# Performance work log

Hardware: AMD Instinct MI355X
Metric: run time of the kernel (lower is better)

## Reference

```python
import jax, jax.numpy as jnp
import numpy as np

NUM_HEADS = 4


def setup_inputs() -> dict:
    key = jax.random.key(0)
    ks = jax.random.split(key, 12)
    N, E_edges, ND, ED, D, G = 50000, 800000, 128, 64, 256, 128
    h = jax.random.normal(ks[0], (N, ND), dtype=jnp.float32)
    edge_index = jax.random.randint(ks[1], (2, E_edges), 0, N)
    edge_attr = jax.random.normal(ks[2], (E_edges, ED), dtype=jnp.float32)
    batch = jnp.sort(jax.random.randint(ks[3], (N,), 0, G))
    node_w = jax.random.normal(ks[4], (D, ND), dtype=jnp.float32) / np.sqrt(ND)
    node_b = jnp.zeros((D,), dtype=jnp.float32)
    edge_w = jax.random.normal(ks[5], (D, ED), dtype=jnp.float32) / np.sqrt(ED)
    edge_b = jnp.zeros((D,), dtype=jnp.float32)
    query = jax.random.normal(ks[6], (1, D), dtype=jnp.float32)
    in_w = jax.random.normal(ks[7], (3 * D, D), dtype=jnp.float32) / np.sqrt(D)
    in_b = jnp.zeros((3 * D,), dtype=jnp.float32)
    out_w = jax.random.normal(ks[8], (D, D), dtype=jnp.float32) / np.sqrt(D)
    out_b = jnp.zeros((D,), dtype=jnp.float32)
    return {"h": h, "edge_index": edge_index, "edge_attr": edge_attr, "batch": batch,
            "num_graphs": G, "node_w": node_w, "node_b": node_b,
            "edge_w": edge_w, "edge_b": edge_b, "query": query,
            "in_w": in_w, "in_b": in_b, "out_w": out_w, "out_b": out_b}


def reference(h, edge_index, edge_attr, batch, num_graphs,
              node_w, node_b, edge_w, edge_b, query, in_w, in_b, out_w, out_b):
    N = h.shape[0]
    D = query.shape[-1]
    dh = D // NUM_HEADS
    G = num_graphs
    # node projection
    h_proj = h @ node_w.T + node_b  # [N, D]
    # scatter-mean edge features to source nodes
    row = edge_index[0]
    e_proj = edge_attr @ edge_w.T + edge_b  # [E, D]
    e_sum = jax.ops.segment_sum(e_proj, row, num_segments=N)
    cnt = jax.ops.segment_sum(jnp.ones((row.shape[0],), jnp.float32), row, num_segments=N)
    h_proj = h_proj + e_sum / jnp.maximum(cnt, 1.0)[:, None]
    # per-graph single-query multi-head attention (torch MultiheadAttention math)
    wq, wk, wv = in_w[:D], in_w[D:2 * D], in_w[2 * D:]
    bq, bk, bv = in_b[:D], in_b[D:2 * D], in_b[2 * D:]
    q = (query @ wq.T + bq).reshape(NUM_HEADS, dh)            # [H, dh]
    k = (h_proj @ wk.T + bk).reshape(N, NUM_HEADS, dh)        # [N, H, dh]
    v = (h_proj @ wv.T + bv).reshape(N, NUM_HEADS, dh)        # [N, H, dh]
    scores = jnp.einsum('hd,nhd->nh', q, k) / jnp.sqrt(jnp.float32(dh))  # [N, H]
    smax = jax.ops.segment_max(scores, batch, num_segments=G)  # [G, H]
    w = jnp.exp(scores - smax[batch])                          # [N, H]
    denom = jax.ops.segment_sum(w, batch, num_segments=G)      # [G, H]
    p = w / jnp.maximum(denom[batch], 1e-30)                   # [N, H]
    pooled = jax.ops.segment_sum(p[:, :, None] * v, batch, num_segments=G)  # [G, H, dh]
    out = pooled.reshape(G, 1, D) @ out_w.T + out_b            # [G, 1, D]
    return out
```

## Files before the change

kernel.cpp:

```cpp
#include <hip/hip_runtime.h>
#include <hip/hip_bf16.h>
#include <math.h>

#define NDIM 128
#define EDIM 64
#define DDIM 256
#define BM 32
#define APK_STRIDE 204
#define HPB_STRIDE 264
#define NSPLIT 4
#define CAP 96
#define NSWZ (8 * 12 * 64 * 8)

typedef __attribute__((ext_vector_type(8))) short short8;
typedef __attribute__((ext_vector_type(16))) float floatx16;

__device__ inline ushort f2bf(float x) {
    uint32_t u = __float_as_uint(x);
    uint32_t r = (u + 0x7fff + ((u >> 16) & 1)) >> 16;
    return (ushort)r;
}
__device__ inline float bf2f(ushort h) { return __uint_as_float(((uint32_t)h) << 16); }
__device__ inline uint32_t pack_hilo(float x) {
    ushort hi = f2bf(x);
    ushort lo = f2bf(x - bf2f(hi));
    return (uint32_t)hi | ((uint32_t)lo << 16);
}

__global__ __launch_bounds__(256) void k_setup(
    int* __restrict__ zero_p, int n_zero, int ZBLK,
    const float* __restrict__ node_w, const float* __restrict__ edge_w,
    ushort* __restrict__ whi, ushort* __restrict__ wlo,
    const float* __restrict__ query, const float* __restrict__ in_w,
    const float* __restrict__ in_b, float* __restrict__ qk, float* __restrict__ sb)
{
    const int tid = threadIdx.x;
    int b = blockIdx.x;
    if (b < ZBLK) {
        int i = b * 256 + tid;
        if (i < n_zero) zero_p[i] = 0;
        return;
    }
    b -= ZBLK;
    if (b < 192) {
        int idx = b * 256 + tid;
        int i = idx & 7;
        int l = (idx >> 3) & 63;
        int rest = idx >> 9;
        int s = rest % 12;
        int t2 = rest / 12;
        int k = s * 16 + (l >> 5) * 8 + i;
        int col = t2 * 32 + (l & 31);
        float val = (k < NDIM) ? node_w[(size_t)col * NDIM + k]
                               : edge_w[(size_t)col * EDIM + (k - NDIM)];
        ushort hi = f2bf(val);
        ushort lo = f2bf(val - bf2f(hi));
        whi[idx] = hi;
        wlo[idx] = lo;
        return;
    }
    __shared__ float q_s[DDIM];
    __shared__ float qv[DDIM];
    q_s[tid] = query[tid];
    __syncthreads();
    float acc = in_b[tid];
    const float* wq = in_w + (size_t)tid * DDIM;
    for (int i = 0; i < DDIM; ++i) acc += q_s[i] * wq[i];
    qv[tid] = acc;
    __syncthreads();
    for (int h = 0; h < 4; ++h) {
        float a = 0.f;
        for (int d = 0; d < 64; ++d)
            a += qv[h * 64 + d] * in_w[(size_t)(DDIM + h * 64 + d) * DDIM + tid];
        qk[h * DDIM + tid] = a;
    }
    if (tid < 4) {
        float a = 0.f;
        for (int d = 0; d < 64; ++d) a += qv[tid * 64 + d] * in_b[DDIM + tid * 64 + d];
        sb[tid] = a;
    }
}

__global__ __launch_bounds__(256) void k_scatter(
    const int* __restrict__ erow, int* __restrict__ fill,
    int* __restrict__ perm, int E)
{
    int e = blockIdx.x * 256 + threadIdx.x;
    if (e < E) {
        int r = erow[e];
        int pos = atomicAdd(&fill[r], 1);
        if (pos < CAP) perm[(size_t)r * CAP + pos] = e;
    }
}

__global__ __launch_bounds__(256) void k_projagg(
    const float* __restrict__ h, const float* __restrict__ edge_attr,
    const int* __restrict__ perm, const int* __restrict__ fill,
    const ushort* __restrict__ whi, const ushort* __restrict__ wlo,
    const float* __restrict__ node_b, const float* __restrict__ edge_b,
    const float* __restrict__ qk, const float* __restrict__ sb,
    ushort* __restrict__ h_proj_bf, float* __restrict__ scores, int N)
{
    extern __shared__ char smem[];
    uint32_t* A_pk = (uint32_t*)smem;
    ushort*   hpbuf = (ushort*)smem;
    __shared__ float qk_s[4 * DDIM];
    __shared__ float cnt_s[BM];
    __shared__ float sb_s[4];

    const int tid = threadIdx.x;
    const int n0 = blockIdx.x * BM;

    if (tid < BM) {
        int n = n0 + tid;
        cnt_s[tid] = (n < N) ? (float)fill[n] : 0.f;
    }
    if (tid < 4) sb_s[tid] = sb[tid];
    for (int i = tid; i < 4 * DDIM; i += 256) qk_s[i] = qk[i];

    const float4* h4 = reinterpret_cast<const float4*>(h);
#pragma unroll
    for (int it = 0; it < 4; ++it) {
        int idx4 = tid + 256 * it;
        int node = idx4 >> 5;
        int kq = idx4 & 31;
        float4 v = make_float4(0.f, 0.f, 0.f, 0.f);
        if (n0 + node < N) v = h4[(size_t)(n0 + node) * 32 + kq];
        uint32_t* dst = &A_pk[node * APK_STRIDE + kq * 4];
        dst[0] = pack_hilo(v.x); dst[1] = pack_hilo(v.y);
        dst[2] = pack_hilo(v.z); dst[3] = pack_hilo(v.w);
    }

    __syncthreads();

    {
        int node = tid >> 3;
        int seg8 = tid & 7;
        int n = n0 + node;
        float a0 = 0.f, a1 = 0.f, a2 = 0.f, a3 = 0.f;
        float a4 = 0.f, a5 = 0.f, a6 = 0.f, a7 = 0.f;
        if (n < N) {
            int s = n * CAP;
            int c = min((int)cnt_s[node], CAP);
            const float* ea = edge_attr + seg8 * 8;
            int j = 0;
            for (; j + 3 < c; j += 4) {
                int e0 = perm[s + j], e1 = perm[s + j + 1];
                int e2 = perm[s + j + 2], e3 = perm[s + j + 3];
                float4 v0a = *reinterpret_cast<const float4*>(ea + (size_t)e0 * EDIM);
                float4 v0b = *reinterpret_cast<const float4*>(ea + (size_t)e0 * EDIM + 4);
                float4 v1a = *reinterpret_cast<const float4*>(ea + (size_t)e1 * EDIM);
                float4 v1b = *reinterpret_cast<const float4*>(ea + (size_t)e1 * EDIM + 4);
                float4 v2a = *reinterpret_cast<const float4*>(ea + (size_t)e2 * EDIM);
                float4 v2b = *reinterpret_cast<const float4*>(ea + (size_t)e2 * EDIM + 4);
                float4 v3a = *reinterpret_cast<const float4*>(ea + (size_t)e3 * EDIM);
                float4 v3b = *reinterpret_cast<const float4*>(ea + (size_t)e3 * EDIM + 4);
                a0 += (v0a.x + v1a.x) + (v2a.x + v3a.x);
                a1 += (v0a.y + v1a.y) + (v2a.y + v3a.y);
                a2 += (v0a.z + v1a.z) + (v2a.z + v3a.z);
                a3 += (v0a.w + v1a.w) + (v2a.w + v3a.w);
                a4 += (v0b.x + v1b.x) + (v2b.x + v3b.x);
                a5 += (v0b.y + v1b.y) + (v2b.y + v3b.y);
                a6 += (v0b.z + v1b.z) + (v2b.z + v3b.z);
                a7 += (v0b.w + v1b.w) + (v2b.w + v3b.w);
            }
            for (; j < c; ++j) {
                int e0 = perm[s + j];
                float4 va = *reinterpret_cast<const float4*>(ea + (size_t)e0 * EDIM);
                float4 vb = *reinterpret_cast<const float4*>(ea + (size_t)e0 * EDIM + 4);
                a0 += va.x; a1 += va.y; a2 += va.z; a3 += va.w;
                a4 += vb.x; a5 += vb.y; a6 += vb.z; a7 += vb.w;
            }
        }
        float inv = 1.f / fmaxf(cnt_s[node], 1.f);
        uint32_t* dst = &A_pk[node * APK_STRIDE + NDIM + seg8 * 8];
        dst[0] = pack_hilo(a0 * inv); dst[1] = pack_hilo(a1 * inv);
        dst[2] = pack_hilo(a2 * inv); dst[3] = pack_hilo(a3 * inv);
        dst[4] = pack_hilo(a4 * inv); dst[5] = pack_hilo(a5 * inv);
        dst[6] = pack_hilo(a6 * inv); dst[7] = pack_hilo(a7 * inv);
    }
    __syncthreads();

    const int lane = tid & 63;
    const int w = tid >> 6;
    const int kg8 = (lane >> 5) * 8;
    const uint32_t* arow_p = &A_pk[(lane & 31) * APK_STRIDE];

    floatx16 acc[2];
#pragma unroll
    for (int t = 0; t < 2; ++t) acc[t] = 0.f;

#pragma unroll 4
    for (int s = 0; s < 12; ++s) {
        uint32_t au[8];
        *reinterpret_cast<uint4*>(&au[0]) = *reinterpret_cast<const uint4*>(&arow_p[s * 16 + kg8]);
        *reinterpret_cast<uint4*>(&au[4]) = *reinterpret_cast<const uint4*>(&arow_p[s * 16 + kg8 + 4]);
        short8 ahi, alo;
#pragma unroll
        for (int j = 0; j < 8; ++j) {
            ahi[j] = (short)(au[j] & 0xffffu);
            alo[j] = (short)(au[j] >> 16);
        }
#pragma unroll
        for (int t = 0; t < 2; ++t) {
            size_t boff = ((size_t)(((w * 2 + t) * 12 + s) * 64) + lane) * 8;
            short8 bhi = *reinterpret_cast<const short8*>(whi + boff);
            short8 blo = *reinterpret_cast<const short8*>(wlo + boff);
            acc[t] = __builtin_amdgcn_mfma_f32_32x32x16_bf16(ahi, bhi, acc[t], 0, 0, 0);
            acc[t] = __builtin_amdgcn_mfma_f32_32x32x16_bf16(ahi, blo, acc[t], 0, 0, 0);
            acc[t] = __builtin_amdgcn_mfma_f32_32x32x16_bf16(alo, bhi, acc[t], 0, 0, 0);
        }
    }
    __syncthreads();

#pragma unroll
    for (int t = 0; t < 2; ++t) {
        int colt = (w * 2 + t) * 32 + (lane & 31);
        float nb = node_b[colt];
        float eb = edge_b[colt];
#pragma unroll
        for (int r = 0; r < 16; ++r) {
            int row = (r & 3) + 8 * (r >> 2) + 4 * (lane >> 5);
            float fl = (cnt_s[row] >= 0.5f) ? 1.f : 0.f;
            float hp = acc[t][r] + nb + fl * eb;
            hpbuf[row * HPB_STRIDE + colt] = f2bf(hp);
        }
    }
    __syncthreads();

    {
        int row = tid >> 3, seg = tid & 7;
        int n = n0 + row;
        float s0 = 0.f, s1 = 0.f, s2 = 0.f, s3 = 0.f;
#pragma unroll
        for (int q = 0; q < 4; ++q) {
            short8 v = *reinterpret_cast<const short8*>(
                &hpbuf[row * HPB_STRIDE + seg * 32 + q * 8]);
#pragma unroll
            for (int jj = 0; jj < 8; ++jj) {
                float hv = bf2f((ushort)v[jj]);
                int dim = seg * 32 + q * 8 + jj;
                s0 += hv * qk_s[0 * DDIM + dim];
                s1 += hv * qk_s[1 * DDIM + dim];
                s2 += hv * qk_s[2 * DDIM + dim];
                s3 += hv * qk_s[3 * DDIM + dim];
            }
            if (n < N)
                *reinterpret_cast<short8*>(
                    &h_proj_bf[(size_t)n * DDIM + seg * 32 + q * 8]) = v;
        }
#pragma unroll
        for (int off = 1; off < 8; off <<= 1) {
            s0 += __shfl_xor(s0, off);
            s1 += __shfl_xor(s1, off);
            s2 += __shfl_xor(s2, off);
            s3 += __shfl_xor(s3, off);
        }
        if (seg == 0 && n < N) {
            scores[(size_t)n * 4 + 0] = (s0 + sb_s[0]) * 0.125f;
            scores[(size_t)n * 4 + 1] = (s1 + sb_s[1]) * 0.125f;
            scores[(size_t)n * 4 + 2] = (s2 + sb_s[2]) * 0.125f;
            scores[(size_t)n * 4 + 3] = (s3 + sb_s[3]) * 0.125f;
        }
    }
}

__global__ __launch_bounds__(256) void k_pool2(
    const ushort* __restrict__ h_proj_bf, const float* __restrict__ scores,
    const int* __restrict__ batch,
    float* __restrict__ pm, float* __restrict__ pd, float* __restrict__ phb, int N)
{
    __shared__ float sc_s[256 * 4];
    __shared__ float red_s[16];
    __shared__ float red[4][4][DDIM];

    const int b = blockIdx.x;
    const int g = b >> 2;
    const int part = b & 3;
    const int tid = threadIdx.x;
    const int lane = tid & 63;
    const int wave = tid >> 6;
    const int ng = tid >> 6;
    const int d0 = (tid & 63) * 4;

    int lo = 0, hi = N;
    while (lo < hi) { int mid = (lo + hi) >> 1; if (batch[mid] < g) lo = mid + 1; else hi = mid; }
    const int s = lo;
    hi = N;
    while (lo < hi) { int mid = (lo + hi) >> 1; if (batch[mid] < g + 1) lo = mid + 1; else hi = mid; }
    const int e = lo;
    const int len = e - s;
    const int cs = s + (len * part) / NSPLIT;
    const int ce = s + (len * (part + 1)) / NSPLIT;

    float m[4], dn[4];
    float hbv[4][4];
#pragma unroll
    for (int hh = 0; hh < 4; ++hh) {
        m[hh] = -INFINITY; dn[hh] = 0.f;
#pragma unroll
        for (int d = 0; d < 4; ++d) hbv[hh][d] = 0.f;
    }

    const int h = tid & 3;

    for (int c = cs; c < ce; c += 256) {
        int cn = min(256, ce - c);
        __syncthreads();
        if (tid < cn)
            *reinterpret_cast<float4*>(&sc_s[tid * 4]) =
                *reinterpret_cast<const float4*>(scores + (size_t)(c + tid) * 4);
        __syncthreads();

        float lm = -INFINITY;
        for (int n = tid >> 2; n < cn; n += 64) lm = fmaxf(lm, sc_s[n * 4 + h]);
#pragma unroll
        for (int off = 4; off < 64; off <<= 1) lm = fmaxf(lm, __shfl_xor(lm, off));
        if (lane < 4) red_s[wave * 4 + lane] = lm;
        __syncthreads();

        float nm[4];
#pragma unroll
        for (int hh = 0; hh < 4; ++hh) {
            float cm = fmaxf(fmaxf(red_s[hh], red_s[4 + hh]),
                             fmaxf(red_s[8 + hh], red_s[12 + hh]));
            nm[hh] = fmaxf(m[hh], cm);
            float sc = expf(m[hh] - nm[hh]);
            dn[hh] *= sc;
#pragma unroll
            for (int d = 0; d < 4; ++d) hbv[hh][d] *= sc;
            m[hh] = nm[hh];
        }
        __syncthreads();

        float mh = (h == 0) ? nm[0] : (h == 1) ? nm[1] : (h == 2) ? nm[2] : nm[3];
        float ld = 0.f;
        for (int idx = tid; idx < cn * 4; idx += 256) {
            float wv = expf(sc_s[idx] - mh);
            sc_s[idx] = wv;
            ld += wv;
        }
#pragma unroll
        for (int off = 4; off < 64; off <<= 1) ld += __shfl_xor(ld, off);
        __syncthreads();
        if (lane < 4) red_s[wave * 4 + lane] = ld;
        __syncthreads();
#pragma unroll
        for (int hh = 0; hh < 4; ++hh)
            dn[hh] += red_s[hh] + red_s[4 + hh] + red_s[8 + hh] + red_s[12 + hh];

#pragma unroll 2
        for (int nb = 0; nb < cn; nb += 4) {
            int ln = nb + ng;
            bool valid = ln < cn;
            float4 w4 = make_float4(0.f, 0.f, 0.f, 0.f);
            ushort4 hv = make_ushort4(0, 0, 0, 0);
            if (valid) {
                w4 = *reinterpret_cast<const float4*>(&sc_s[ln * 4]);
                hv = *reinterpret_cast<const ushort4*>(
                    &h_proj_bf[(size_t)(c + ln) * DDIM + d0]);
            }
            float vx = bf2f(hv.x), vy = bf2f(hv.y), vz = bf2f(hv.z), vw = bf2f(hv.w);
            hbv[0][0] += w4.x * vx; hbv[1][0] += w4.y * vx; hbv[2][0] += w4.z * vx; hbv[3][0] += w4.w * vx;
            hbv[0][1] += w4.x * vy; hbv[1][1] += w4.y * vy; hbv[2][1] += w4.z * vy; hbv[3][1] += w4.w * vy;
            hbv[0][2] += w4.x * vz; hbv[1][2] += w4.y * vz; hbv[2][2] += w4.z * vz; hbv[3][2] += w4.w * vz;
            hbv[0][3] += w4.x * vw; hbv[1][3] += w4.y * vw; hbv[2][3] += w4.z * vw; hbv[3][3] += w4.w * vw;
        }
    }

    __syncthreads();
#pragma unroll
    for (int hh = 0; hh < 4; ++hh)
#pragma unroll
        for (int d = 0; d < 4; ++d)
            red[ng][hh][d0 + d] = hbv[hh][d];
    __syncthreads();

    if (tid < 4) { pm[b * 4 + tid] = m[tid]; pd[b * 4 + tid] = dn[tid]; }
#pragma unroll
    for (int hh = 0; hh < 4; ++hh)
        phb[(size_t)(b * 4 + hh) * DDIM + tid] =
            red[0][hh][tid] + red[1][hh][tid] + red[2][hh][tid] + red[3][hh][tid];
}

__global__ __launch_bounds__(256) void k_out(
    const float* __restrict__ pm, const float* __restrict__ pd, const float* __restrict__ phb,
    const float* __restrict__ in_w, const float* __restrict__ in_b,
    const float* __restrict__ out_w, const float* __restrict__ out_b,
    float* __restrict__ out)
{
    __shared__ float hb_s[4 * DDIM];
    __shared__ float po_s[DDIM];

    const int g = blockIdx.x;
    const int tid = threadIdx.x;
    const int b0 = NSPLIT * g;

    float M[4], dnm[4], sc[NSPLIT][4];
#pragma unroll
    for (int hh = 0; hh < 4; ++hh) {
        float Mh = -INFINITY;
#pragma unroll
        for (int p = 0; p < NSPLIT; ++p) Mh = fmaxf(Mh, pm[(b0 + p) * 4 + hh]);
        M[hh] = Mh;
        float d = 0.f;
#pragma unroll
        for (int p = 0; p < NSPLIT; ++p) {
            float mp = pm[(b0 + p) * 4 + hh];
            float scp = (mp == -INFINITY) ? 0.f : expf(mp - Mh);
            sc[p][hh] = scp;
            d += pd[(b0 + p) * 4 + hh] * scp;
        }
        dnm[hh] = d;
    }
    const float has = (M[0] > -INFINITY) ? 1.f : 0.f;

#pragma unroll
    for (int hh = 0; hh < 4; ++hh) {
        float hb = 0.f;
#pragma unroll
        for (int p = 0; p < NSPLIT; ++p)
            hb += phb[(size_t)((b0 + p) * 4 + hh) * DDIM + tid] * sc[p][hh];
        hb_s[hh * DDIM + tid] = hb / fmaxf(dnm[hh], 1e-30f);
    }
    __syncthreads();

    const int jh = tid >> 6;
    const float* wv_row = in_w + (size_t)(2 * DDIM + tid) * DDIM;
    const float* hbr = &hb_s[jh * DDIM];
    float p = 0.f;
    for (int i = 0; i < DDIM; i += 4) {
        float4 a = *reinterpret_cast<const float4*>(hbr + i);
        float4 bb = *reinterpret_cast<const float4*>(wv_row + i);
        p += a.x * bb.x + a.y * bb.y + a.z * bb.z + a.w * bb.w;
    }
    p = (p + in_b[2 * DDIM + tid]) * has;
    po_s[tid] = p;
    __syncthreads();

    const float* ow_row = out_w + (size_t)tid * DDIM;
    float o = out_b[tid];
    for (int i = 0; i < DDIM; i += 4) {
        float4 a = *reinterpret_cast<const float4*>(&po_s[i]);
        float4 bb = *reinterpret_cast<const float4*>(ow_row + i);
        o += a.x * bb.x + a.y * bb.y + a.z * bb.z + a.w * bb.w;
    }
    out[(size_t)g * DDIM + tid] = o;
}

extern "C" void kernel_launch(void* const* d_in, const int* in_sizes, int n_in,
                              void* d_out, int out_size, void* d_ws, size_t ws_size,
                              hipStream_t stream) {
    const float* h         = (const float*)d_in[0];
    const int*   edge_idx  = (const int*)d_in[1];
    const float* edge_attr = (const float*)d_in[2];
    const int*   batch     = (const int*)d_in[3];
    const float* node_w    = (const float*)d_in[5];
    const float* node_b    = (const float*)d_in[6];
    const float* edge_w    = (const float*)d_in[7];
    const float* edge_b    = (const float*)d_in[8];
    const float* query     = (const float*)d_in[9];
    const float* in_w      = (const float*)d_in[10];
    const float* in_b      = (const float*)d_in[11];
    const float* out_w     = (const float*)d_in[12];
    const float* out_b     = (const float*)d_in[13];
    float* out = (float*)d_out;

    const int N = in_sizes[0] / NDIM;
    const int E = in_sizes[2] / EDIM;
    const int G = out_size / DDIM;

    char* ws = (char*)d_ws;
    size_t off = 0;
    auto alloc = [&](size_t bytes) { void* p = ws + off; off += (bytes + 255) & ~(size_t)255; return p; };

    int*    fill       = (int*)alloc((size_t)N * 4);
    int*    perm       = (int*)alloc((size_t)N * CAP * 4);
    ushort* h_proj_bf  = (ushort*)alloc((size_t)N * DDIM * 2);
    float*  scores     = (float*)alloc((size_t)N * 4 * 4);
    ushort* whi        = (ushort*)alloc((size_t)NSWZ * 2);
    ushort* wlo        = (ushort*)alloc((size_t)NSWZ * 2);
    float*  qk         = (float*)alloc(4 * DDIM * 4);
    float*  sb         = (float*)alloc(16 * 4);
    float*  pm         = (float*)alloc((size_t)NSPLIT * G * 4 * 4);
    float*  pd         = (float*)alloc((size_t)NSPLIT * G * 4 * 4);
    float*  phb        = (float*)alloc((size_t)NSPLIT * G * 4 * DDIM * 4);

    const int ZBLK = (N + 255) / 256;
    k_setup<<<ZBLK + 192 + 1, 256, 0, stream>>>(
        fill, N, ZBLK, node_w, edge_w, whi, wlo, query, in_w, in_b, qk, sb);

    k_scatter<<<(E + 255) / 256, 256, 0, stream>>>(edge_idx, fill, perm, E);

    const int ldsA = BM * APK_STRIDE * 4;
    k_projagg<<<(N + BM - 1) / BM, 256, ldsA, stream>>>(
        h, edge_attr, perm, fill, whi, wlo, node_b, edge_b, qk, sb,
        h_proj_bf, scores, N);

    k_pool2<<<NSPLIT * G, 256, 0, stream>>>(h_proj_bf, scores, batch, pm, pd, phb, N);
    k_out<<<G, 256, 0, stream>>>(pm, pd, phb, in_w, in_b, out_w, out_b, out);
}
```

Measured before the change: 209.3 us.

## Scatter edge features into per-node bf16 bins instead of index permutation

The scatter kernel now copies each edge's feature row, converted to bf16, straight into a per-node bin at its atomically claimed slot. This replaces the old edge-index permutation list. The aggregation kernel then reads contiguous bf16 rows per node instead of gathering fp32 rows through indirection. The goal is to swap random fp32 gathers in the projection kernel for streaming scatter-writes plus coalesced reads at half the bytes. In exchange it adds a large bin buffer (N*CAP*64*2 bytes), an extra write pass of edge data, and bf16 rounding of the edge features before they are summed.

```diff
diff --git a/kernel.cpp b/kernel.cpp
--- a/kernel.cpp
+++ b/kernel.cpp
@@ -81,21 +81,34 @@
     }
 }
 
-__global__ __launch_bounds__(256) void k_scatter(
-    const int* __restrict__ erow, int* __restrict__ fill,
-    int* __restrict__ perm, int E)
+__global__ __launch_bounds__(256) void k_scatbin(
+    const int* __restrict__ erow, const float* __restrict__ edge_attr,
+    int* __restrict__ fill, ushort* __restrict__ ebin, int E)
 {
-    int e = blockIdx.x * 256 + threadIdx.x;
-    if (e < E) {
-        int r = erow[e];
-        int pos = atomicAdd(&fill[r], 1);
-        if (pos < CAP) perm[(size_t)r * CAP + pos] = e;
-    }
+    int gid = blockIdx.x * 256 + threadIdx.x;
+    int e = gid >> 3;
+    int seg8 = gid & 7;
+    if (e >= E) return;
+    int r = erow[e];
+    int pos = 0;
+    if (seg8 == 0) pos = atomicAdd(&fill[r], 1);
+    pos = __shfl(pos, 0, 8);
+    if (pos >= CAP) return;
+    const float* ea = edge_attr + (size_t)e * EDIM + seg8 * 8;
+    float4 va = *reinterpret_cast<const float4*>(ea);
+    float4 vb = *reinterpret_cast<const float4*>(ea + 4);
+    short8 o;
+    o[0] = (short)f2bf(va.x); o[1] = (short)f2bf(va.y);
+    o[2] = (short)f2bf(va.z); o[3] = (short)f2bf(va.w);
+    o[4] = (short)f2bf(vb.x); o[5] = (short)f2bf(vb.y);
+    o[6] = (short)f2bf(vb.z); o[7] = (short)f2bf(vb.w);
+    *reinterpret_cast<short8*>(
+        ebin + ((size_t)r * CAP + pos) * EDIM + seg8 * 8) = o;
 }
 
 __global__ __launch_bounds__(256) void k_projagg(
-    const float* __restrict__ h, const float* __restrict__ edge_attr,
-    const int* __restrict__ perm, const int* __restrict__ fill,
+    const float* __restrict__ h, const ushort* __restrict__ ebin,
+    const int* __restrict__ fill,
     const ushort* __restrict__ whi, const ushort* __restrict__ wlo,
     const float* __restrict__ node_b, const float* __restrict__ edge_b,
     const float* __restrict__ qk, const float* __restrict__ sb,
@@ -137,47 +150,33 @@
         int node = tid >> 3;
         int seg8 = tid & 7;
         int n = n0 + node;
-        float a0 = 0.f, a1 = 0.f, a2 = 0.f, a3 = 0.f;
-        float a4 = 0.f, a5 = 0.f, a6 = 0.f, a7 = 0.f;
+        float a[8];
+#pragma unroll
+        for (int i = 0; i < 8; ++i) a[i] = 0.f;
         if (n < N) {
-            int s = n * CAP;
             int c = min((int)cnt_s[node], CAP);
-            const float* ea = edge_attr + seg8 * 8;
+            const ushort* eb = ebin + ((size_t)n * CAP) * EDIM + seg8 * 8;
             int j = 0;
             for (; j + 3 < c; j += 4) {
-                int e0 = perm[s + j], e1 = perm[s + j + 1];
-                int e2 = perm[s + j + 2], e3 = perm[s + j + 3];
-                float4 v0a = *reinterpret_cast<const float4*>(ea + (size_t)e0 * EDIM);
-                float4 v0b = *reinterpret_cast<const float4*>(ea + (size_t)e0 * EDIM + 4);
-                float4 v1a = *reinterpret_cast<const float4*>(ea + (size_t)e1 * EDIM);
-                float4 v1b = *reinterpret_cast<const float4*>(ea + (size_t)e1 * EDIM + 4);
-                float4 v2a = *reinterpret_cast<const float4*>(ea + (size_t)e2 * EDIM);
-                float4 v2b = *reinterpret_cast<const float4*>(ea + (size_t)e2 * EDIM + 4);
-                float4 v3a = *reinterpret_cast<const float4*>(ea + (size_t)e3 * EDIM);
-                float4 v3b = *reinterpret_cast<const float4*>(ea + (size_t)e3 * EDIM + 4);
-                a0 += (v0a.x + v1a.x) + (v2a.x + v3a.x);
-                a1 += (v0a.y + v1a.y) + (v2a.y + v3a.y);
-                a2 += (v0a.z + v1a.z) + (v2a.z + v3a.z);
-                a3 += (v0a.w + v1a.w) + (v2a.w + v3a.w);
-                a4 += (v0b.x + v1b.x) + (v2b.x + v3b.x);
-                a5 += (v0b.y + v1b.y) + (v2b.y + v3b.y);
-                a6 += (v0b.z + v1b.z) + (v2b.z + v3b.z);
-                a7 += (v0b.w + v1b.w) + (v2b.w + v3b.w);
+                short8 v0 = *reinterpret_cast<const short8*>(eb + (size_t)(j + 0) * EDIM);
+                short8 v1 = *reinterpret_cast<const short8*>(eb + (size_t)(j + 1) * EDIM);
+                short8 v2 = *reinterpret_cast<const short8*>(eb + (size_t)(j + 2) * EDIM);
+                short8 v3 = *reinterpret_cast<const short8*>(eb + (size_t)(j + 3) * EDIM);
+#pragma unroll
+                for (int i = 0; i < 8; ++i)
+                    a[i] += (bf2f((ushort)v0[i]) + bf2f((ushort)v1[i]))
+                          + (bf2f((ushort)v2[i]) + bf2f((ushort)v3[i]));
             }
             for (; j < c; ++j) {
-                int e0 = perm[s + j];
-                float4 va = *reinterpret_cast<const float4*>(ea + (size_t)e0 * EDIM);
-                float4 vb = *reinterpret_cast<const float4*>(ea + (size_t)e0 * EDIM + 4);
-                a0 += va.x; a1 += va.y; a2 += va.z; a3 += va.w;
-                a4 += vb.x; a5 += vb.y; a6 += vb.z; a7 += vb.w;
+                short8 v0 = *reinterpret_cast<const short8*>(eb + (size_t)j * EDIM);
+#pragma unroll
+                for (int i = 0; i < 8; ++i) a[i] += bf2f((ushort)v0[i]);
             }
         }
         float inv = 1.f / fmaxf(cnt_s[node], 1.f);
         uint32_t* dst = &A_pk[node * APK_STRIDE + NDIM + seg8 * 8];
-        dst[0] = pack_hilo(a0 * inv); dst[1] = pack_hilo(a1 * inv);
-        dst[2] = pack_hilo(a2 * inv); dst[3] = pack_hilo(a3 * inv);
-        dst[4] = pack_hilo(a4 * inv); dst[5] = pack_hilo(a5 * inv);
-        dst[6] = pack_hilo(a6 * inv); dst[7] = pack_hilo(a7 * inv);
+#pragma unroll
+        for (int i = 0; i < 8; ++i) dst[i] = pack_hilo(a[i] * inv);
     }
     __syncthreads();
 
@@ -475,7 +474,6 @@
     auto alloc = [&](size_t bytes) { void* p = ws + off; off += (bytes + 255) & ~(size_t)255; return p; };
 
     int*    fill       = (int*)alloc((size_t)N * 4);
-    int*    perm       = (int*)alloc((size_t)N * CAP * 4);
     ushort* h_proj_bf  = (ushort*)alloc((size_t)N * DDIM * 2);
     float*  scores     = (float*)alloc((size_t)N * 4 * 4);
     ushort* whi        = (ushort*)alloc((size_t)NSWZ * 2);
@@ -485,16 +483,18 @@
     float*  pm         = (float*)alloc((size_t)NSPLIT * G * 4 * 4);
     float*  pd         = (float*)alloc((size_t)NSPLIT * G * 4 * 4);
     float*  phb        = (float*)alloc((size_t)NSPLIT * G * 4 * DDIM * 4);
+    ushort* ebin       = (ushort*)alloc((size_t)N * CAP * EDIM * 2);
 
     const int ZBLK = (N + 255) / 256;
     k_setup<<<ZBLK + 192 + 1, 256, 0, stream>>>(
         fill, N, ZBLK, node_w, edge_w, whi, wlo, query, in_w, in_b, qk, sb);
 
-    k_scatter<<<(E + 255) / 256, 256, 0, stream>>>(edge_idx, fill, perm, E);
+    k_scatbin<<<((E * 8) + 255) / 256, 256, 0, stream>>>(
+        edge_idx, edge_attr, fill, ebin, E);
 
     const int ldsA = BM * APK_STRIDE * 4;
     k_projagg<<<(N + BM - 1) / BM, 256, ldsA, stream>>>(
-        h, edge_attr, perm, fill, whi, wlo, node_b, edge_b, qk, sb,
+        h, ebin, fill, whi, wlo, node_b, edge_b, qk, sb,
         h_proj_bf, scores, N);
 
     k_pool2<<<NSPLIT * G, 256, 0, stream>>>(h_proj_bf, scores, batch, pm, pd, phb, N);
```

Result: no change. 211.9 us (+1.3%).
